# Kernel optimization log

Measured on AMD Instinct MI355X. Metric: run time of the kernel, lower is better.

## Reference

```python
import jax, jax.numpy as jnp
import numpy as np

WIN = 9  # window_size from init


def _box_filter_3d(x, k):
    """Separable normalized box filter over the 3 spatial dims of NCDHW x.
    Mathematically identical to a dense k^3 mean filter with SAME padding."""
    c = x.shape[1]
    pad = k // 2
    for axis in range(3):
        kshape = [1, 1, 1]
        kshape[axis] = k
        kern = jnp.ones((c, 1, *kshape), x.dtype) / k  # depthwise, normalized per-axis
        padding = [(pad, pad) if a == axis else (0, 0) for a in range(3)]
        x = jax.lax.conv_general_dilated(
            x, kern, window_strides=(1, 1, 1), padding=padding,
            dimension_numbers=('NCDHW', 'OIDHW', 'NCDHW'),
            feature_group_count=c)
    return x


def setup_inputs() -> dict:
    key = jax.random.key(0)
    k1, k2 = jax.random.split(key)
    shape = (1, 1, 192, 192, 192)
    pred = jax.random.uniform(k1, shape, dtype=jnp.float32)
    target = jax.random.uniform(k2, shape, dtype=jnp.float32)
    return {"pred": pred, "target": target}


def reference(pred, target):
    Ii, Ji = target, pred
    # local means of I, J, I^2, J^2, IJ via one grouped (5-channel) box filter
    all_five = jnp.concatenate([Ii, Ji, Ii * Ii, Ji * Ji, Ii * Ji], axis=1)
    f = _box_filter_3d(all_five, WIN)
    mu1, mu2 = f[:, 0:1], f[:, 1:2]
    conv_I2, conv_J2, conv_IJ = f[:, 2:3], f[:, 3:4], f[:, 4:5]
    sigma1_sq = conv_I2 - mu1 * mu1
    sigma2_sq = conv_J2 - mu2 * mu2
    sigma12 = conv_IJ - mu1 * mu2
    eps = jnp.finfo(sigma12.dtype).eps
    cc = sigma12 * sigma12 / (sigma1_sq * sigma2_sq + eps)
    return 1.0 - jnp.mean(cc)
```

## Files before the change

kernel.cpp:

```cpp
#include <hip/hip_runtime.h>
#include <hip/hip_bf16.h>

#define SDIM 192
#define S2 (SDIM*SDIM)
#define S3 ((size_t)SDIM*S2)
#define NCH 5
#define RAD 4

#define STRH 8
#define RROW 16
#define RQU 224
#define WSTR 96
#define NSTRIP (SDIM/STRH)
#define SQQ(Q) ((Q) + ((Q) >> 3))

#define KB_THR 128
#define KB_KBC 4
#define KB_POSB (S2/(KB_THR*KB_KBC))
#define KB_DCH 8
#define KB_NDC (SDIM/KB_DCH)
#define KB_GRID (KB_POSB*KB_NDC)
#define NPART KB_GRID

typedef float v2f __attribute__((ext_vector_type(2)));

__device__ __forceinline__ unsigned packbf(float lo, float hi) {
    __hip_bfloat162 h2 = __float22bfloat162_rn(make_float2(lo, hi));
    unsigned u; __builtin_memcpy(&u, &h2, 4); return u;
}
__device__ __forceinline__ float ulo(unsigned u) { return __uint_as_float(u << 16); }
__device__ __forceinline__ float uhi(unsigned u) { return __uint_as_float(u & 0xffff0000u); }

__global__ __launch_bounds__(256) void ka_wh(const float* __restrict__ pred,
                                             const float* __restrict__ tgt,
                                             unsigned* __restrict__ BU) {
    const int b = blockIdx.x;
    const int strip = b % NSTRIP;
    const int d = b / NSTRIP;
    const int h0 = strip * STRH;
    const size_t dbase = (size_t)d * S2;
    const int t = threadIdx.x;

    __shared__ unsigned IJ[RROW][RQU];
    __shared__ unsigned wfU[NCH][RROW][WSTR];

    if (t < RROW * 8) {
        const int r = t >> 3, p = t & 7;
        const int col = (p < 4) ? p : (216 + p);
        IJ[r][col] = 0u;
    }
    const float4* tg4 = (const float4*)tgt;
    const float4* pr4 = (const float4*)pred;
#pragma unroll
    for (int it = 0; it < 3; ++it) {
        const int u = t + 256 * it;
        const int r = u / 48, q = u % 48;
        const int hh = h0 - RAD + r;
        float4 vi = make_float4(0.f, 0.f, 0.f, 0.f), vj = vi;
        if (hh >= 0 && hh < SDIM) {
            const size_t gi = (dbase + (size_t)hh * SDIM) / 4 + q;
            vi = tg4[gi]; vj = pr4[gi];
        }
        uint4 w;
        w.x = packbf(vi.x, vj.x); w.y = packbf(vi.y, vj.y);
        w.z = packbf(vi.z, vj.z); w.w = packbf(vi.w, vj.w);
        *(uint4*)&IJ[r][4 * SQQ(q + 1)] = w;
    }
    __syncthreads();

#pragma unroll
    for (int it = 0; it < 2; ++it) {
        const int u = t + 256 * it;
        if (u < (RROW / 2) * 48) {
            const int rp = u / 48, cu = u % 48;
            const int row0 = 2 * rp, row1 = row0 + 1;
            const uint4 a0 = *(const uint4*)&IJ[row0][4 * SQQ(cu)];
            const uint4 b0 = *(const uint4*)&IJ[row0][4 * SQQ(cu + 1)];
            const uint4 c0 = *(const uint4*)&IJ[row0][4 * SQQ(cu + 2)];
            const uint4 a1 = *(const uint4*)&IJ[row1][4 * SQQ(cu)];
            const uint4 b1 = *(const uint4*)&IJ[row1][4 * SQQ(cu + 1)];
            const uint4 c1 = *(const uint4*)&IJ[row1][4 * SQQ(cu + 2)];
            unsigned r0[12] = {a0.x, a0.y, a0.z, a0.w, b0.x, b0.y, b0.z, b0.w,
                               c0.x, c0.y, c0.z, c0.w};
            unsigned r1[12] = {a1.x, a1.y, a1.z, a1.w, b1.x, b1.y, b1.z, b1.w,
                               c1.x, c1.y, c1.z, c1.w};
            v2f fi[12], fj[12];
#pragma unroll
            for (int k = 0; k < 12; ++k) {
                fi[k] = (v2f){ulo(r0[k]), ulo(r1[k])};
                fj[k] = (v2f){uhi(r0[k]), uhi(r1[k])};
            }

#define W4P(CH, EXPR) { \
            v2f pv[12]; \
            _Pragma("unroll") for (int k = 0; k < 12; ++k) pv[k] = (EXPR); \
            v2f s0 = pv[0]; \
            _Pragma("unroll") for (int k = 1; k < 9; ++k) s0 += pv[k]; \
            const v2f s1 = s0 - pv[0] + pv[9]; \
            const v2f s2 = s1 - pv[1] + pv[10]; \
            const v2f s3 = s2 - pv[2] + pv[11]; \
            uint2 o0; o0.x = packbf(s0.x, s1.x); o0.y = packbf(s2.x, s3.x); \
            *(uint2*)&wfU[CH][row0][2 * cu] = o0; \
            uint2 o1; o1.x = packbf(s0.y, s1.y); o1.y = packbf(s2.y, s3.y); \
            *(uint2*)&wfU[CH][row1][2 * cu] = o1; }

            W4P(0, fi[k])
            W4P(1, fj[k])
            W4P(2, fi[k] * fi[k])
            W4P(3, fj[k] * fj[k])
            W4P(4, fi[k] * fj[k])
#undef W4P
        }
    }
    __syncthreads();

#pragma unroll
    for (int it = 0; it < 2; ++it) {
        const int col = t + 256 * it;
        if (col < NCH * 96) {
            const int c = col / 96, wp = col % 96;
            v2f vh[RROW];
#pragma unroll
            for (int r = 0; r < RROW; ++r) {
                const unsigned v = wfU[c][r][wp];
                vh[r] = (v2f){ulo(v), uhi(v)};
            }
            v2f s = vh[0];
#pragma unroll
            for (int r = 1; r < 9; ++r) s += vh[r];
            unsigned* dst = BU + (size_t)c * (S3 / 2) + (dbase + (size_t)h0 * SDIM) / 2 + wp;
            dst[0] = packbf(s.x, s.y);
#pragma unroll
            for (int hr = 1; hr < STRH; ++hr) {
                s += vh[hr + 8] - vh[hr - 1];
                dst[hr * (SDIM / 2)] = packbf(s.x, s.y);
            }
        }
    }
}

#define SLICE2(s, OP) { const size_t sb = ((size_t)(s) * S2 + pos0) >> 2; \
    _Pragma("unroll") for (int c = 0; c < NCH; ++c) { \
        const uint2 v = B2[(size_t)c * (S3 >> 2) + sb]; \
        z[c][0] OP ulo(v.x); z[c][1] OP uhi(v.x); \
        z[c][2] OP ulo(v.y); z[c][3] OP uhi(v.y); } }

__global__ __launch_bounds__(KB_THR) void kb_d_cc(const unsigned* __restrict__ BU,
                                                  float* __restrict__ partials) {
    const int bid = blockIdx.x;
    const int dc = bid / KB_POSB;
    const int pb = bid % KB_POSB;
    const int d0 = dc * KB_DCH;
    const int pos0 = pb * (KB_THR * KB_KBC) + threadIdx.x * KB_KBC;
    const uint2* B2 = (const uint2*)BU;

    float z[NCH][KB_KBC];
#pragma unroll
    for (int c = 0; c < NCH; ++c)
#pragma unroll
        for (int i = 0; i < KB_KBC; ++i) z[c][i] = 0.f;

#pragma unroll
    for (int dd = -RAD; dd <= RAD; ++dd) {
        const int s = d0 + dd;
        if (s >= 0 && s < SDIM) SLICE2(s, +=)
    }

    const float inv = 1.0f / 729.0f;
    const float eps = 1.1920929e-07f;
    float acc = 0.f;

#pragma unroll
    for (int k = 0; k < KB_DCH; ++k) {
        const int d = d0 + k;
#pragma unroll
        for (int i = 0; i < KB_KBC; ++i) {
            const float mu1 = z[0][i] * inv;
            const float mu2 = z[1][i] * inv;
            const float sg1 = z[2][i] * inv - mu1 * mu1;
            const float sg2 = z[3][i] * inv - mu2 * mu2;
            const float s12 = z[4][i] * inv - mu1 * mu2;
            acc += (s12 * s12) * __builtin_amdgcn_rcpf(sg1 * sg2 + eps);
        }
        const int da = d + RAD + 1;
        const int ds = d - RAD;
        if (da < SDIM) SLICE2(da, +=)
        if (ds >= 0)   SLICE2(ds, -=)
    }

    __shared__ float red[KB_THR];
    red[threadIdx.x] = acc;
    __syncthreads();
#pragma unroll
    for (int o = KB_THR / 2; o > 0; o >>= 1) {
        if (threadIdx.x < o) red[threadIdx.x] += red[threadIdx.x + o];
        __syncthreads();
    }
    if (threadIdx.x == 0) partials[bid] = red[0];
}

__global__ __launch_bounds__(256) void k4_finalize(const float* __restrict__ partials,
                                                   float* __restrict__ out) {
    __shared__ float sm[256];
    float s = 0.f;
    for (int i = threadIdx.x; i < NPART; i += 256) s += partials[i];
    sm[threadIdx.x] = s;
    __syncthreads();
#pragma unroll
    for (int o = 128; o > 0; o >>= 1) {
        if (threadIdx.x < o) sm[threadIdx.x] += sm[threadIdx.x + o];
        __syncthreads();
    }
    if (threadIdx.x == 0) out[0] = 1.0f - sm[0] / (float)((size_t)SDIM * S2);
}

extern "C" void kernel_launch(void* const* d_in, const int* in_sizes, int n_in,
                              void* d_out, int out_size, void* d_ws, size_t ws_size,
                              hipStream_t stream) {
    const float* pred = (const float*)d_in[0];
    const float* tgt  = (const float*)d_in[1];
    float* out = (float*)d_out;

    const size_t b_bytes = (size_t)NCH * S3 * sizeof(__hip_bfloat16);
    const size_t b_pad = (b_bytes + 255) & ~(size_t)255;

    unsigned* BU = (unsigned*)d_ws;
    float* partials = (float*)((char*)d_ws + b_pad);

    ka_wh<<<SDIM * NSTRIP, 256, 0, stream>>>(pred, tgt, BU);
    kb_d_cc<<<KB_GRID, KB_THR, 0, stream>>>(BU, partials);
    k4_finalize<<<1, 256, 0, stream>>>(partials, out);
}
```

Baseline: 72.74 us.

## Widen vertical-pass stores with nontemporal hints, shrink depth-pass blocks to one wave

The vertical box-sum stage now has each thread handle two adjacent column pairs. It reads 8-byte words from shared memory and writes 8-byte bfloat16 pairs with nontemporal stores, where it used to make 4-byte stores over two loop iterations. The depth-sum kernel drops to 64 threads per block, so the block is a single wavefront, and it replaces the shared-memory tree reduction and its barriers with wave shuffles. This is meant to cut store instruction count, reduce cache pollution from the large intermediate buffer, and remove synchronization overhead. In exchange it doubles the number of depth-pass blocks and partials, and the nontemporal hint may slow the next kernel's reads of that buffer.

```diff
diff --git a/kernel.cpp b/kernel.cpp
--- a/kernel.cpp
+++ b/kernel.cpp
@@ -14,7 +14,7 @@
 #define NSTRIP (SDIM/STRH)
 #define SQQ(Q) ((Q) + ((Q) >> 3))
 
-#define KB_THR 128
+#define KB_THR 64
 #define KB_KBC 4
 #define KB_POSB (S2/(KB_THR*KB_KBC))
 #define KB_DCH 8
@@ -23,6 +23,7 @@
 #define NPART KB_GRID
 
 typedef float v2f __attribute__((ext_vector_type(2)));
+typedef unsigned v2u __attribute__((ext_vector_type(2)));
 
 __device__ __forceinline__ unsigned packbf(float lo, float hi) {
     __hip_bfloat162 h2 = __float22bfloat162_rn(make_float2(lo, hi));
@@ -114,27 +115,28 @@
     }
     __syncthreads();
 
-#pragma unroll
-    for (int it = 0; it < 2; ++it) {
-        const int col = t + 256 * it;
-        if (col < NCH * 96) {
-            const int c = col / 96, wp = col % 96;
-            v2f vh[RROW];
-#pragma unroll
-            for (int r = 0; r < RROW; ++r) {
-                const unsigned v = wfU[c][r][wp];
-                vh[r] = (v2f){ulo(v), uhi(v)};
-            }
-            v2f s = vh[0];
-#pragma unroll
-            for (int r = 1; r < 9; ++r) s += vh[r];
-            unsigned* dst = BU + (size_t)c * (S3 / 2) + (dbase + (size_t)h0 * SDIM) / 2 + wp;
-            dst[0] = packbf(s.x, s.y);
-#pragma unroll
-            for (int hr = 1; hr < STRH; ++hr) {
-                s += vh[hr + 8] - vh[hr - 1];
-                dst[hr * (SDIM / 2)] = packbf(s.x, s.y);
-            }
+    if (t < NCH * 48) {
+        const int c = t / 48, wpp = t % 48;
+        v2f va[RROW], vb[RROW];
+#pragma unroll
+        for (int r = 0; r < RROW; ++r) {
+            const uint2 v = *(const uint2*)&wfU[c][r][2 * wpp];
+            va[r] = (v2f){ulo(v.x), uhi(v.x)};
+            vb[r] = (v2f){ulo(v.y), uhi(v.y)};
+        }
+        v2f sa = va[0], sb = vb[0];
+#pragma unroll
+        for (int r = 1; r < 9; ++r) { sa += va[r]; sb += vb[r]; }
+        unsigned* dst = BU + (size_t)c * (S3 / 2) + (dbase + (size_t)h0 * SDIM) / 2 + 2 * wpp;
+        v2u o;
+        o.x = packbf(sa.x, sa.y); o.y = packbf(sb.x, sb.y);
+        __builtin_nontemporal_store(o, (v2u*)dst);
+#pragma unroll
+        for (int hr = 1; hr < STRH; ++hr) {
+            sa += va[hr + 8] - va[hr - 1];
+            sb += vb[hr + 8] - vb[hr - 1];
+            o.x = packbf(sa.x, sa.y); o.y = packbf(sb.x, sb.y);
+            __builtin_nontemporal_store(o, (v2u*)(dst + hr * (SDIM / 2)));
         }
     }
 }
@@ -188,15 +190,10 @@
         if (ds >= 0)   SLICE2(ds, -=)
     }
 
-    __shared__ float red[KB_THR];
-    red[threadIdx.x] = acc;
-    __syncthreads();
-#pragma unroll
-    for (int o = KB_THR / 2; o > 0; o >>= 1) {
-        if (threadIdx.x < o) red[threadIdx.x] += red[threadIdx.x + o];
-        __syncthreads();
-    }
-    if (threadIdx.x == 0) partials[bid] = red[0];
+#pragma unroll
+    for (int off = 32; off > 0; off >>= 1)
+        acc += __shfl_down(acc, off, 64);
+    if (threadIdx.x == 0) partials[bid] = acc;
 }
 
 __global__ __launch_bounds__(256) void k4_finalize(const float* __restrict__ partials,
```

Result: slower. 80.05 us (+10.0%).
